# Kernel optimization log

Measured on AMD Instinct MI355X. Metric: run time of the kernel, lower is better.

The kernel has to match this reference:

```python
import jax, jax.numpy as jnp
import numpy as np

LTH_THOLD = 0.0

def _mlp(x, w1, b1, w2, b2, w3, b3):
    # x: [b,h,s,d]; w*: [h,in,out]; per-head 3-layer MLP with SiLU
    h1 = jax.nn.silu(jnp.einsum('bhsd,hde->bhse', x, w1) + b1[None, :, None, :])
    h2 = jax.nn.silu(jnp.einsum('bhsd,hde->bhse', h1, w2) + b2[None, :, None, :])
    return jnp.einsum('bhsd,hde->bhse', h2, w3) + b3[None, :, None, :]

def setup_inputs() -> dict:
    key = jax.random.key(0)
    ks = jax.random.split(key, 16)
    b, h, s, d, idim, fdim = 2, 32, 2048, 128, 128, 32
    sc1 = 1.0 / np.sqrt(d); sc2 = 1.0 / np.sqrt(idim)
    def lin(k, fan_in, shape, sc):
        return jax.random.uniform(k, shape, jnp.float32, -sc, sc)
    inp = {
        'K': jax.random.normal(ks[0], (b, h, s, d), jnp.float32),
        'Q': jax.random.normal(ks[1], (b, h, s, d), jnp.float32),
        'wk1': lin(ks[2], d, (h, d, idim), sc1), 'bk1': lin(ks[3], d, (h, idim), sc1),
        'wk2': lin(ks[4], idim, (h, idim, idim), sc2), 'bk2': lin(ks[5], idim, (h, idim), sc2),
        'wk3': lin(ks[6], idim, (h, idim, fdim), sc2), 'bk3': lin(ks[7], idim, (h, fdim), sc2),
        'wq1': lin(ks[8], d, (h, d, idim), sc1), 'bq1': lin(ks[9], d, (h, idim), sc1),
        'wq2': lin(ks[10], idim, (h, idim, idim), sc2), 'bq2': lin(ks[11], idim, (h, idim), sc2),
        'wq3': lin(ks[12], idim, (h, idim, fdim), sc2), 'bq3': lin(ks[13], idim, (h, fdim), sc2),
    }
    return inp

def reference(K, Q, wk1, bk1, wk2, bk2, wk3, bk3, wq1, bq1, wq2, bq2, wq3, bq3):
    Klift = jnp.tanh(_mlp(K, wk1, bk1, wk2, bk2, wk3, bk3))  # [b,h,sk,32]
    Qlift = jnp.tanh(_mlp(Q, wq1, bq1, wq2, bq2, wq3, bq3))  # [b,h,sq,32]
    scores = jnp.einsum('bhtd,bhsd->bhts', Qlift, Klift)      # [b,h,sq,sk]
    sq, sk = Qlift.shape[2], Klift.shape[2]
    causal = jnp.tril(jnp.ones((sq, sk), bool), k=sk - sq)
    mask_value = jnp.finfo(scores.dtype).min
    scores = jnp.where(causal[None, None], scores, mask_value)
    scores = jax.nn.sigmoid(scores - LTH_THOLD)
    return (scores, Klift)
```

## Files before the change

kernel.cpp:

```cpp
#include <hip/hip_runtime.h>

typedef __attribute__((ext_vector_type(8))) short bf16x8;
typedef __attribute__((ext_vector_type(4))) float f32x4;

#define MFMA(a,b,c) __builtin_amdgcn_mfma_f32_16x16x32_bf16(a,b,c,0,0,0)

static __device__ __forceinline__ unsigned short f2bf(float f){
  unsigned u = __float_as_uint(f);
  u += 0x7FFF + ((u>>16)&1);
  return (unsigned short)(u>>16);
}
static __device__ __forceinline__ float bf2f(unsigned short b){
  return __uint_as_float(((unsigned)b)<<16);
}

__global__ __launch_bounds__(256) void wswz(
    const float* __restrict__ wk1, const float* __restrict__ wk2, const float* __restrict__ wk3,
    const float* __restrict__ wq1, const float* __restrict__ wq2, const float* __restrict__ wq3,
    unsigned short* __restrict__ wb)
{
  int y = blockIdx.y;
  int net = y / 3, layer = y % 3;
  const float* src = net ? (layer==0?wq1: layer==1?wq2:wq3)
                         : (layer==0?wk1: layer==1?wk2:wk3);
  int N  = (layer==2) ? 32 : 128;
  int NT = N / 16;
  int total = 32 * NT * 4 * 64;
  int e = blockIdx.x * 256 + threadIdx.x;
  if (e >= total) return;
  int lane = e & 63;
  int ks   = (e >> 6) & 3;
  int nt   = (e >> 8) % NT;
  int h    = (e >> 8) / NT;
  int k0 = ks*32 + 8*(lane>>4);
  int n0 = nt*16 + (lane&15);
  const float* s = src + (size_t)h*128*N + (size_t)k0*N + n0;
  unsigned short hi[8], lo[8];
  #pragma unroll
  for (int j=0;j<8;++j){
    float v = s[(size_t)j*N];
    unsigned short hh = f2bf(v);
    hi[j] = hh;
    lo[j] = f2bf(v - bf2f(hh));
  }
  size_t nb   = (size_t)net * 2359296;
  size_t loff = (layer==0) ? 0 : (layer==1) ? 1048576 : 2097152;
  size_t losz = (layer==2) ? 131072 : 524288;
  size_t eidx = ((((size_t)h*NT + nt)*4 + ks)*64 + lane)*8;
  unsigned short* dH = wb + nb + loff + eidx;
  unsigned short* dL = dH + losz;
  *(bf16x8*)dH = *(const bf16x8*)hi;
  *(bf16x8*)dL = *(const bf16x8*)lo;
}

__global__ __launch_bounds__(256,3) void lift(
    const float* __restrict__ Kin, const float* __restrict__ Qin,
    const float* __restrict__ bk1, const float* __restrict__ bk2, const float* __restrict__ bk3,
    const float* __restrict__ bq1, const float* __restrict__ bq2, const float* __restrict__ bq3,
    const unsigned short* __restrict__ wb,
    unsigned short* __restrict__ qlift, unsigned short* __restrict__ klift,
    float* __restrict__ kout)
{
  __shared__ unsigned short XH[64][136];
  __shared__ unsigned short XL[64][136];
  int bid = blockIdx.x;
  int h   = (bid & 7)*4 + ((bid>>3)&3);
  int st  = (bid>>5) & 31;
  int bb  = (bid>>10) & 1;
  int net = bid>>11;
  size_t rowbase = (size_t)(bb*32 + h)*2048 + (size_t)st*64;
  const float* X = (net ? Qin : Kin) + rowbase*128;
  const unsigned short* wn = wb + (size_t)net*2359296;
  const float* b1 = (net ? bq1 : bk1) + h*128;
  const float* b2 = (net ? bq2 : bk2) + h*128;
  const float* b3 = (net ? bq3 : bk3) + h*32;
  unsigned short* lifto = net ? qlift : klift;

  int tid = threadIdx.x, w = tid >> 6, l = tid & 63;
  int lr = l & 15, lg = l >> 4;
  int acol0 = 8*lg;

  #pragma unroll
  for (int i=0;i<8;++i){
    int row = i*8 + (tid>>5);
    int col = (tid&31)*4;
    float4 v = *(const float4*)&X[(size_t)row*128 + col];
    unsigned u0=__float_as_uint(v.x), u1=__float_as_uint(v.y),
             u2=__float_as_uint(v.z), u3=__float_as_uint(v.w);
    float l0 = v.x - __uint_as_float(u0 & 0xFFFF0000u);
    float l1 = v.y - __uint_as_float(u1 & 0xFFFF0000u);
    float l2 = v.z - __uint_as_float(u2 & 0xFFFF0000u);
    float l3 = v.w - __uint_as_float(u3 & 0xFFFF0000u);
    *(uint2*)&XH[row][col] = make_uint2((u0>>16) | (u1 & 0xFFFF0000u),
                                        (u2>>16) | (u3 & 0xFFFF0000u));
    *(uint2*)&XL[row][col] = make_uint2((__float_as_uint(l0)>>16) | (__float_as_uint(l1) & 0xFFFF0000u),
                                        (__float_as_uint(l2)>>16) | (__float_as_uint(l3) & 0xFFFF0000u));
  }
  __syncthreads();

  for (int L=0; L<2; ++L){
    const unsigned short* wH = wn + (size_t)L*1048576;
    const unsigned short* wL = wH + 524288;
    const float* bias = L ? b2 : b1;
    f32x4 acc[2][4];
    #pragma unroll
    for (int ntl=0;ntl<2;++ntl)
      #pragma unroll
      for (int rt=0;rt<4;++rt)
        acc[ntl][rt] = (f32x4){0.f,0.f,0.f,0.f};

    #pragma unroll
    for (int ks=0;ks<4;++ks){
      bf16x8 bh[2], bl[2];
      #pragma unroll
      for (int ntl=0;ntl<2;++ntl){
        size_t eidx = ((((size_t)h*8 + (w*2+ntl))*4 + ks)*64 + l)*8;
        bh[ntl] = *(const bf16x8*)(wH + eidx);
        bl[ntl] = *(const bf16x8*)(wL + eidx);
      }
      #pragma unroll
      for (int rt=0;rt<4;++rt){
        bf16x8 ah = *(const bf16x8*)&XH[rt*16+lr][ks*32 + acol0];
        bf16x8 al = *(const bf16x8*)&XL[rt*16+lr][ks*32 + acol0];
        #pragma unroll
        for (int ntl=0;ntl<2;++ntl){
          f32x4 a = acc[ntl][rt];
          a = MFMA(bh[ntl], ah, a);
          a = MFMA(bh[ntl], al, a);
          a = MFMA(bl[ntl], ah, a);
          acc[ntl][rt] = a;
        }
      }
    }
    __syncthreads();
    #pragma unroll
    for (int ntl=0;ntl<2;++ntl){
      int n0 = (w*2+ntl)*16 + 4*lg;
      float4 bv = *(const float4*)&bias[n0];
      float bvv[4] = {bv.x, bv.y, bv.z, bv.w};
      #pragma unroll
      for (int rt=0;rt<4;++rt){
        int row = rt*16 + lr;
        unsigned hh[4], ll[4];
        #pragma unroll
        for (int i=0;i<4;++i){
          float v = acc[ntl][rt][i] + bvv[i];
          float sg = v * __builtin_amdgcn_rcpf(1.f + __expf(-v));
          unsigned u = __float_as_uint(sg);
          hh[i] = u >> 16;
          float lo = sg - __uint_as_float(u & 0xFFFF0000u);
          ll[i] = __float_as_uint(lo) >> 16;
        }
        *(uint2*)&XH[row][n0] = make_uint2(hh[0] | (hh[1]<<16), hh[2] | (hh[3]<<16));
        *(uint2*)&XL[row][n0] = make_uint2(ll[0] | (ll[1]<<16), ll[2] | (ll[3]<<16));
      }
    }
    __syncthreads();
  }

  {
    const unsigned short* wH = wn + 2097152;
    const unsigned short* wL = wH + 131072;
    int nt = w >> 1;
    int rb = (w & 1) * 2;
    f32x4 acc3[2];
    acc3[0] = (f32x4){0.f,0.f,0.f,0.f};
    acc3[1] = (f32x4){0.f,0.f,0.f,0.f};
    #pragma unroll
    for (int ks=0;ks<4;++ks){
      size_t eidx = ((((size_t)h*2 + nt)*4 + ks)*64 + l)*8;
      bf16x8 bh = *(const bf16x8*)(wH + eidx);
      bf16x8 bl = *(const bf16x8*)(wL + eidx);
      #pragma unroll
      for (int j=0;j<2;++j){
        bf16x8 ah = *(const bf16x8*)&XH[(rb+j)*16+lr][ks*32 + acol0];
        bf16x8 al = *(const bf16x8*)&XL[(rb+j)*16+lr][ks*32 + acol0];
        f32x4 a = acc3[j];
        a = MFMA(bh, ah, a);
        a = MFMA(bh, al, a);
        a = MFMA(bl, ah, a);
        acc3[j] = a;
      }
    }
    int n0 = nt*16 + 4*lg;
    float4 bv = *(const float4*)&b3[n0];
    float bvv[4] = {bv.x, bv.y, bv.z, bv.w};
    #pragma unroll
    for (int j=0;j<2;++j){
      int row = (rb+j)*16 + lr;
      float t4[4];
      unsigned short hb[4];
      #pragma unroll
      for (int i=0;i<4;++i){
        float v = acc3[j][i] + bvv[i];
        float e2 = __expf(2.f*v);
        float t  = 1.f - 2.f*__builtin_amdgcn_rcpf(e2 + 1.f);
        t4[i] = t;
        hb[i] = f2bf(t);
      }
      size_t gro = (rowbase + (size_t)row)*32 + n0;
      *(uint2*)&lifto[gro] = make_uint2((unsigned)hb[0] | ((unsigned)hb[1]<<16),
                                        (unsigned)hb[2] | ((unsigned)hb[3]<<16));
      if (net == 0)
        *(float4*)&kout[gro] = make_float4(t4[0], t4[1], t4[2], t4[3]);
    }
  }
}

__global__ __launch_bounds__(256) void scores_k(
    const unsigned short* __restrict__ qlift,
    const unsigned short* __restrict__ klift,
    float* __restrict__ out)
{
  int bid = blockIdx.x;
  int tc = bid & 15, tr = (bid >> 4) & 15, bh = bid >> 8;
  size_t sbase = (size_t)bh * 2048 * 2048;
  int r0 = tr * 128, c0 = tc * 128;
  int tid = threadIdx.x;

  if (tc > tr){
    float4 z = {0.f,0.f,0.f,0.f};
    #pragma unroll
    for (int it=0; it<16; ++it){
      int idx = it*256 + tid;
      int row = idx >> 5, c4 = idx & 31;
      *(float4*)&out[sbase + (size_t)(r0+row)*2048 + c0 + c4*4] = z;
    }
    return;
  }

  int w = tid >> 6, l = tid & 63;
  int lr = l & 15, lg = l >> 4;
  int acol0 = 8*lg;
  const unsigned short* qb = qlift + ((size_t)bh*2048 + r0 + w*32)*32;
  bf16x8 q0 = *(const bf16x8*)(qb + (size_t)lr*32 + acol0);
  bf16x8 q1 = *(const bf16x8*)(qb + (size_t)(16+lr)*32 + acol0);
  bool diag = (tc == tr);
  int t0 = r0 + w*32 + lr;
  int t1 = t0 + 16;

  const unsigned short* kb = klift + ((size_t)bh*2048 + c0)*32;
  bf16x8 kf[8];
  #pragma unroll
  for (int st8=0; st8<8; ++st8)
    kf[st8] = *(const bf16x8*)(kb + (size_t)(st8*16+lr)*32 + acol0);

  #pragma unroll
  for (int st8=0; st8<8; ++st8){
    f32x4 z4 = {0.f,0.f,0.f,0.f};
    f32x4 s0 = MFMA(kf[st8], q0, z4);
    f32x4 s1 = MFMA(kf[st8], q1, z4);
    int scol = c0 + st8*16 + 4*lg;
    f32x4 p0, p1;
    #pragma unroll
    for (int i=0;i<4;++i){
      float v0 = s0[i];
      float pv0 = __builtin_amdgcn_rcpf(1.f + __expf(-v0));
      if (diag && (scol + i > t0)) pv0 = 0.f;
      p0[i] = pv0;
      float v1 = s1[i];
      float pv1 = __builtin_amdgcn_rcpf(1.f + __expf(-v1));
      if (diag && (scol + i > t1)) pv1 = 0.f;
      p1[i] = pv1;
    }
    *(f32x4*)&out[sbase + (size_t)t0*2048 + scol] = p0;
    *(f32x4*)&out[sbase + (size_t)t1*2048 + scol] = p1;
  }
}

extern "C" void kernel_launch(void* const* d_in, const int* in_sizes, int n_in,
                              void* d_out, int out_size, void* d_ws, size_t ws_size,
                              hipStream_t stream) {
  const float* K   = (const float*)d_in[0];
  const float* Q   = (const float*)d_in[1];
  const float* wk1 = (const float*)d_in[2];  const float* bk1 = (const float*)d_in[3];
  const float* wk2 = (const float*)d_in[4];  const float* bk2 = (const float*)d_in[5];
  const float* wk3 = (const float*)d_in[6];  const float* bk3 = (const float*)d_in[7];
  const float* wq1 = (const float*)d_in[8];  const float* bq1 = (const float*)d_in[9];
  const float* wq2 = (const float*)d_in[10]; const float* bq2 = (const float*)d_in[11];
  const float* wq3 = (const float*)d_in[12]; const float* bq3 = (const float*)d_in[13];
  float* out = (float*)d_out;

  unsigned short* ws    = (unsigned short*)d_ws;
  unsigned short* qlift = ws;
  unsigned short* klift = ws + 4194304;
  unsigned short* wbase = ws + 8388608;

  hipLaunchKernelGGL(wswz, dim3(256,6), dim3(256), 0, stream,
                     wk1, wk2, wk3, wq1, wq2, wq3, wbase);
  hipLaunchKernelGGL(lift, dim3(4096), dim3(256), 0, stream,
                     K, Q, bk1, bk2, bk3, bq1, bq2, bq3,
                     wbase, qlift, klift, out + 268435456ull);
  hipLaunchKernelGGL(scores_k, dim3(16384), dim3(256), 0, stream,
                     qlift, klift, out);
}
```

Before: 318.1 us.

## Process two row tiles per lift block and prefetch the second tile into registers

Each lift block now handles 128 rows as two 64-row tiles, halving the grid. The second tile's input is loaded into registers before the first tile's MLP runs, so its global-load latency overlaps with compute. It also amortizes per-block setup and weight fetches across two tiles. The cost is 32 extra float registers per thread for the prefetch buffer, which may hurt occupancy at launch bounds (256,3), and the grid is half as large.

```diff
diff --git a/kernel.cpp b/kernel.cpp
--- a/kernel.cpp
+++ b/kernel.cpp
@@ -65,11 +65,11 @@
   __shared__ unsigned short XL[64][136];
   int bid = blockIdx.x;
   int h   = (bid & 7)*4 + ((bid>>3)&3);
-  int st  = (bid>>5) & 31;
-  int bb  = (bid>>10) & 1;
-  int net = bid>>11;
-  size_t rowbase = (size_t)(bb*32 + h)*2048 + (size_t)st*64;
-  const float* X = (net ? Qin : Kin) + rowbase*128;
+  int st2 = (bid>>5) & 15;
+  int bb  = (bid>>9) & 1;
+  int net = bid>>10;
+  size_t rowbase0 = (size_t)(bb*32 + h)*2048 + (size_t)st2*128;
+  const float* X0 = (net ? Qin : Kin) + rowbase0*128;
   const unsigned short* wn = wb + (size_t)net*2359296;
   const float* b1 = (net ? bq1 : bk1) + h*128;
   const float* b2 = (net ? bq2 : bk2) + h*128;
@@ -79,130 +79,162 @@
   int tid = threadIdx.x, w = tid >> 6, l = tid & 63;
   int lr = l & 15, lg = l >> 4;
   int acol0 = 8*lg;
+  int srow = (tid>>5);
+  int scol = (tid&31)*4;
 
   #pragma unroll
   for (int i=0;i<8;++i){
-    int row = i*8 + (tid>>5);
-    int col = (tid&31)*4;
-    float4 v = *(const float4*)&X[(size_t)row*128 + col];
+    int row = i*8 + srow;
+    float4 v = *(const float4*)&X0[(size_t)row*128 + scol];
     unsigned u0=__float_as_uint(v.x), u1=__float_as_uint(v.y),
              u2=__float_as_uint(v.z), u3=__float_as_uint(v.w);
     float l0 = v.x - __uint_as_float(u0 & 0xFFFF0000u);
     float l1 = v.y - __uint_as_float(u1 & 0xFFFF0000u);
     float l2 = v.z - __uint_as_float(u2 & 0xFFFF0000u);
     float l3 = v.w - __uint_as_float(u3 & 0xFFFF0000u);
-    *(uint2*)&XH[row][col] = make_uint2((u0>>16) | (u1 & 0xFFFF0000u),
-                                        (u2>>16) | (u3 & 0xFFFF0000u));
-    *(uint2*)&XL[row][col] = make_uint2((__float_as_uint(l0)>>16) | (__float_as_uint(l1) & 0xFFFF0000u),
-                                        (__float_as_uint(l2)>>16) | (__float_as_uint(l3) & 0xFFFF0000u));
+    *(uint2*)&XH[row][scol] = make_uint2((u0>>16) | (u1 & 0xFFFF0000u),
+                                         (u2>>16) | (u3 & 0xFFFF0000u));
+    *(uint2*)&XL[row][scol] = make_uint2((__float_as_uint(l0)>>16) | (__float_as_uint(l1) & 0xFFFF0000u),
+                                         (__float_as_uint(l2)>>16) | (__float_as_uint(l3) & 0xFFFF0000u));
   }
   __syncthreads();
 
-  for (int L=0; L<2; ++L){
-    const unsigned short* wH = wn + (size_t)L*1048576;
-    const unsigned short* wL = wH + 524288;
-    const float* bias = L ? b2 : b1;
-    f32x4 acc[2][4];
-    #pragma unroll
-    for (int ntl=0;ntl<2;++ntl)
-      #pragma unroll
-      for (int rt=0;rt<4;++rt)
-        acc[ntl][rt] = (f32x4){0.f,0.f,0.f,0.f};
-
-    #pragma unroll
-    for (int ks=0;ks<4;++ks){
-      bf16x8 bh[2], bl[2];
+  float4 binp[8];
+  #pragma unroll
+  for (int i=0;i<8;++i){
+    int row = 64 + i*8 + srow;
+    binp[i] = *(const float4*)&X0[(size_t)row*128 + scol];
+  }
+
+  #pragma unroll 1
+  for (int tile=0; tile<2; ++tile){
+    size_t rowbase = rowbase0 + (size_t)(tile*64);
+    if (tile == 1){
+      __syncthreads();
+      #pragma unroll
+      for (int i=0;i<8;++i){
+        int row = i*8 + srow;
+        float4 v = binp[i];
+        unsigned u0=__float_as_uint(v.x), u1=__float_as_uint(v.y),
+                 u2=__float_as_uint(v.z), u3=__float_as_uint(v.w);
+        float l0 = v.x - __uint_as_float(u0 & 0xFFFF0000u);
+        float l1 = v.y - __uint_as_float(u1 & 0xFFFF0000u);
+        float l2 = v.z - __uint_as_float(u2 & 0xFFFF0000u);
+        float l3 = v.w - __uint_as_float(u3 & 0xFFFF0000u);
+        *(uint2*)&XH[row][scol] = make_uint2((u0>>16) | (u1 & 0xFFFF0000u),
+                                             (u2>>16) | (u3 & 0xFFFF0000u));
+        *(uint2*)&XL[row][scol] = make_uint2((__float_as_uint(l0)>>16) | (__float_as_uint(l1) & 0xFFFF0000u),
+                                             (__float_as_uint(l2)>>16) | (__float_as_uint(l3) & 0xFFFF0000u));
+      }
+      __syncthreads();
+    }
+
+    for (int L=0; L<2; ++L){
+      const unsigned short* wH = wn + (size_t)L*1048576;
+      const unsigned short* wL = wH + 524288;
+      const float* bias = L ? b2 : b1;
+      f32x4 acc[2][4];
+      #pragma unroll
+      for (int ntl=0;ntl<2;++ntl)
+        #pragma unroll
+        for (int rt=0;rt<4;++rt)
+          acc[ntl][rt] = (f32x4){0.f,0.f,0.f,0.f};
+
+      #pragma unroll
+      for (int ks=0;ks<4;++ks){
+        bf16x8 bh[2], bl[2];
+        #pragma unroll
+        for (int ntl=0;ntl<2;++ntl){
+          size_t eidx = ((((size_t)h*8 + (w*2+ntl))*4 + ks)*64 + l)*8;
+          bh[ntl] = *(const bf16x8*)(wH + eidx);
+          bl[ntl] = *(const bf16x8*)(wL + eidx);
+        }
+        #pragma unroll
+        for (int rt=0;rt<4;++rt){
+          bf16x8 ah = *(const bf16x8*)&XH[rt*16+lr][ks*32 + acol0];
+          bf16x8 al = *(const bf16x8*)&XL[rt*16+lr][ks*32 + acol0];
+          #pragma unroll
+          for (int ntl=0;ntl<2;++ntl){
+            f32x4 a = acc[ntl][rt];
+            a = MFMA(bh[ntl], ah, a);
+            a = MFMA(bh[ntl], al, a);
+            a = MFMA(bl[ntl], ah, a);
+            acc[ntl][rt] = a;
+          }
+        }
+      }
+      __syncthreads();
       #pragma unroll
       for (int ntl=0;ntl<2;++ntl){
-        size_t eidx = ((((size_t)h*8 + (w*2+ntl))*4 + ks)*64 + l)*8;
-        bh[ntl] = *(const bf16x8*)(wH + eidx);
-        bl[ntl] = *(const bf16x8*)(wL + eidx);
-      }
-      #pragma unroll
-      for (int rt=0;rt<4;++rt){
-        bf16x8 ah = *(const bf16x8*)&XH[rt*16+lr][ks*32 + acol0];
-        bf16x8 al = *(const bf16x8*)&XL[rt*16+lr][ks*32 + acol0];
-        #pragma unroll
-        for (int ntl=0;ntl<2;++ntl){
-          f32x4 a = acc[ntl][rt];
-          a = MFMA(bh[ntl], ah, a);
-          a = MFMA(bh[ntl], al, a);
-          a = MFMA(bl[ntl], ah, a);
-          acc[ntl][rt] = a;
-        }
-      }
-    }
-    __syncthreads();
-    #pragma unroll
-    for (int ntl=0;ntl<2;++ntl){
-      int n0 = (w*2+ntl)*16 + 4*lg;
-      float4 bv = *(const float4*)&bias[n0];
+        int n0 = (w*2+ntl)*16 + 4*lg;
+        float4 bv = *(const float4*)&bias[n0];
+        float bvv[4] = {bv.x, bv.y, bv.z, bv.w};
+        #pragma unroll
+        for (int rt=0;rt<4;++rt){
+          int row = rt*16 + lr;
+          unsigned hh[4], ll[4];
+          #pragma unroll
+          for (int i=0;i<4;++i){
+            float v = acc[ntl][rt][i] + bvv[i];
+            float sg = v * __builtin_amdgcn_rcpf(1.f + __expf(-v));
+            unsigned u = __float_as_uint(sg);
+            hh[i] = u >> 16;
+            float lo = sg - __uint_as_float(u & 0xFFFF0000u);
+            ll[i] = __float_as_uint(lo) >> 16;
+          }
+          *(uint2*)&XH[row][n0] = make_uint2(hh[0] | (hh[1]<<16), hh[2] | (hh[3]<<16));
+          *(uint2*)&XL[row][n0] = make_uint2(ll[0] | (ll[1]<<16), ll[2] | (ll[3]<<16));
+        }
+      }
+      __syncthreads();
+    }
+
+    {
+      const unsigned short* wH = wn + 2097152;
+      const unsigned short* wL = wH + 131072;
+      int nt = w >> 1;
+      int rb = (w & 1) * 2;
+      f32x4 acc3[2];
+      acc3[0] = (f32x4){0.f,0.f,0.f,0.f};
+      acc3[1] = (f32x4){0.f,0.f,0.f,0.f};
+      #pragma unroll
+      for (int ks=0;ks<4;++ks){
+        size_t eidx = ((((size_t)h*2 + nt)*4 + ks)*64 + l)*8;
+        bf16x8 bh = *(const bf16x8*)(wH + eidx);
+        bf16x8 bl = *(const bf16x8*)(wL + eidx);
+        #pragma unroll
+        for (int j=0;j<2;++j){
+          bf16x8 ah = *(const bf16x8*)&XH[(rb+j)*16+lr][ks*32 + acol0];
+          bf16x8 al = *(const bf16x8*)&XL[(rb+j)*16+lr][ks*32 + acol0];
+          f32x4 a = acc3[j];
+          a = MFMA(bh, ah, a);
+          a = MFMA(bh, al, a);
+          a = MFMA(bl, ah, a);
+          acc3[j] = a;
+        }
+      }
+      int n0 = nt*16 + 4*lg;
+      float4 bv = *(const float4*)&b3[n0];
       float bvv[4] = {bv.x, bv.y, bv.z, bv.w};
       #pragma unroll
-      for (int rt=0;rt<4;++rt){
-        int row = rt*16 + lr;
-        unsigned hh[4], ll[4];
+      for (int j=0;j<2;++j){
+        int row = (rb+j)*16 + lr;
+        float t4[4];
+        unsigned short hb[4];
         #pragma unroll
         for (int i=0;i<4;++i){
-          float v = acc[ntl][rt][i] + bvv[i];
-          float sg = v * __builtin_amdgcn_rcpf(1.f + __expf(-v));
-          unsigned u = __float_as_uint(sg);
-          hh[i] = u >> 16;
-          float lo = sg - __uint_as_float(u & 0xFFFF0000u);
-          ll[i] = __float_as_uint(lo) >> 16;
-        }
-        *(uint2*)&XH[row][n0] = make_uint2(hh[0] | (hh[1]<<16), hh[2] | (hh[3]<<16));
-        *(uint2*)&XL[row][n0] = make_uint2(ll[0] | (ll[1]<<16), ll[2] | (ll[3]<<16));
-      }
-    }
-    __syncthreads();
-  }
-
-  {
-    const unsigned short* wH = wn + 2097152;
-    const unsigned short* wL = wH + 131072;
-    int nt = w >> 1;
-    int rb = (w & 1) * 2;
-    f32x4 acc3[2];
-    acc3[0] = (f32x4){0.f,0.f,0.f,0.f};
-    acc3[1] = (f32x4){0.f,0.f,0.f,0.f};
-    #pragma unroll
-    for (int ks=0;ks<4;++ks){
-      size_t eidx = ((((size_t)h*2 + nt)*4 + ks)*64 + l)*8;
-      bf16x8 bh = *(const bf16x8*)(wH + eidx);
-      bf16x8 bl = *(const bf16x8*)(wL + eidx);
-      #pragma unroll
-      for (int j=0;j<2;++j){
-        bf16x8 ah = *(const bf16x8*)&XH[(rb+j)*16+lr][ks*32 + acol0];
-        bf16x8 al = *(const bf16x8*)&XL[(rb+j)*16+lr][ks*32 + acol0];
-        f32x4 a = acc3[j];
-        a = MFMA(bh, ah, a);
-        a = MFMA(bh, al, a);
-        a = MFMA(bl, ah, a);
-        acc3[j] = a;
-      }
-    }
-    int n0 = nt*16 + 4*lg;
-    float4 bv = *(const float4*)&b3[n0];
-    float bvv[4] = {bv.x, bv.y, bv.z, bv.w};
-    #pragma unroll
-    for (int j=0;j<2;++j){
-      int row = (rb+j)*16 + lr;
-      float t4[4];
-      unsigned short hb[4];
-      #pragma unroll
-      for (int i=0;i<4;++i){
-        float v = acc3[j][i] + bvv[i];
-        float e2 = __expf(2.f*v);
-        float t  = 1.f - 2.f*__builtin_amdgcn_rcpf(e2 + 1.f);
-        t4[i] = t;
-        hb[i] = f2bf(t);
-      }
-      size_t gro = (rowbase + (size_t)row)*32 + n0;
-      *(uint2*)&lifto[gro] = make_uint2((unsigned)hb[0] | ((unsigned)hb[1]<<16),
-                                        (unsigned)hb[2] | ((unsigned)hb[3]<<16));
-      if (net == 0)
-        *(float4*)&kout[gro] = make_float4(t4[0], t4[1], t4[2], t4[3]);
+          float v = acc3[j][i] + bvv[i];
+          float e2 = __expf(2.f*v);
+          float t  = 1.f - 2.f*__builtin_amdgcn_rcpf(e2 + 1.f);
+          t4[i] = t;
+          hb[i] = f2bf(t);
+        }
+        size_t gro = (rowbase + (size_t)row)*32 + n0;
+        *(uint2*)&lifto[gro] = make_uint2((unsigned)hb[0] | ((unsigned)hb[1]<<16),
+                                          (unsigned)hb[2] | ((unsigned)hb[3]<<16));
+        if (net == 0)
+          *(float4*)&kout[gro] = make_float4(t4[0], t4[1], t4[2], t4[3]);
+      }
     }
   }
 }
@@ -288,7 +320,7 @@
 
   hipLaunchKernelGGL(wswz, dim3(256,6), dim3(256), 0, stream,
                      wk1, wk2, wk3, wq1, wq2, wq3, wbase);
-  hipLaunchKernelGGL(lift, dim3(4096), dim3(256), 0, stream,
+  hipLaunchKernelGGL(lift, dim3(2048), dim3(256), 0, stream,
                      K, Q, bk1, bk2, bk3, bq1, bq2, bq3,
                      wbase, qlift, klift, out + 268435456ull);
   hipLaunchKernelGGL(scores_k, dim3(16384), dim3(256), 0, stream,
```

Result: slower. 421.6 us (+32.5%).
